# Kernel tuning notes

Hardware: AMD Instinct MI355X
Metric: run time of the kernel (lower is better)

The kernel has to match this reference:

```python
import jax, jax.numpy as jnp
import numpy as np

N, D, H = 4096, 1024, 16
DK = D // H

def setup_inputs() -> dict:
    key = jax.random.key(0)
    k1, k2 = jax.random.split(key)
    X = jax.random.normal(k1, (N, D), dtype=jnp.float32)
    # torch nn.Linear(D, 2D, bias=False): weight [2D, D]; y = x @ W.T. Store as [D, 2D].
    Wqkv = jax.random.normal(k2, (D, 2 * D), dtype=jnp.float32) * (1.0 / np.sqrt(D))
    return {"X": X, "Wqkv": Wqkv}

def reference(X, Wqkv):
    n = X.shape[0]
    proj = X @ Wqkv                      # [N, 2D]
    qk, v = jnp.split(proj, 2, axis=-1)  # each [N, D]
    qk = qk.reshape(n, H, DK)
    v = v.reshape(n, H, DK)
    scale = DK ** 0.5
    scores = jnp.einsum('nhd,mhd->hnm', qk, qk) / scale  # [H, N, N], Q == K
    att = jax.nn.softmax(scores, axis=-1)
    out = jnp.einsum('hnm,mhd->nhd', att, v)              # [N, H, DK]
    return out.reshape(n, D)
```

## Files before the change

kernel.cpp:

```cpp
#include <hip/hip_runtime.h>

typedef unsigned short u16;
typedef unsigned int u32;
typedef __bf16 bf16x8 __attribute__((ext_vector_type(8)));
typedef float f32x4 __attribute__((ext_vector_type(4)));
typedef float f32x16 __attribute__((ext_vector_type(16)));
typedef int i32x2 __attribute__((ext_vector_type(2)));
typedef unsigned int u32x4 __attribute__((ext_vector_type(4)));

#define N_TOK 4096
#define DMODEL 1024
#define NH 16
#define DKH 64

__device__ inline u16 f2bf(float f){
  unsigned u = __float_as_uint(f);
  u += 0x7fffu + ((u >> 16) & 1u);
  return (u16)(u >> 16);
}

__device__ inline float fexp2(float x){ return __builtin_amdgcn_exp2f(x); }

__global__ __launch_bounds__(256) void k_convX(const float* __restrict__ X, u16* __restrict__ Xb){
  int i = blockIdx.x*256 + threadIdx.x;
  const float4 v = reinterpret_cast<const float4*>(X)[i];
  ushort4 o; o.x=f2bf(v.x); o.y=f2bf(v.y); o.z=f2bf(v.z); o.w=f2bf(v.w);
  reinterpret_cast<ushort4*>(Xb)[i] = o;
}

__global__ __launch_bounds__(256) void k_convW(const float* __restrict__ W, u16* __restrict__ Wt){
  __shared__ float tile[64][65];
  const int bn = blockIdx.x*64;
  const int bk = blockIdx.y*64;
  const int t = threadIdx.x;
  const int c4 = (t & 15)*4;
  const int r  = t >> 4;
  #pragma unroll
  for (int i=0;i<4;i++){
    int k = r + i*16;
    const float4 v = *reinterpret_cast<const float4*>(&W[(size_t)(bk+k)*2048 + bn + c4]);
    tile[k][c4+0]=v.x; tile[k][c4+1]=v.y; tile[k][c4+2]=v.z; tile[k][c4+3]=v.w;
  }
  __syncthreads();
  #pragma unroll
  for (int i=0;i<4;i++){
    int n = r + i*16;
    ushort4 o;
    o.x = f2bf(tile[c4+0][n]);
    o.y = f2bf(tile[c4+1][n]);
    o.z = f2bf(tile[c4+2][n]);
    o.w = f2bf(tile[c4+3][n]);
    *reinterpret_cast<ushort4*>(&Wt[(size_t)(bn+n)*1024 + bk + c4]) = o;
  }
}

__global__ __launch_bounds__(256) void k_gemm(const u16* __restrict__ A, const u16* __restrict__ B,
                                              u16* __restrict__ kf_g, u16* __restrict__ vf_g){
  __shared__ alignas(16) u16 As[128*64];
  __shared__ alignas(16) u16 Bs[128*64];
  const int bm = blockIdx.y*128, bn = blockIdx.x*128;
  const int tid = threadIdx.x, wid = tid>>6, lane = tid&63;
  const int wr = wid>>1, wc = wid&1;
  const int lr = lane&15, lg = lane>>4;
  f32x4 acc[4][4] = {};

  for (int kk=0; kk<DMODEL; kk+=64){
    __syncthreads();
    #pragma unroll
    for (int i=0;i<4;i++){
      const int chunk = (wid*4+i)*64 + lane;
      const int row = chunk>>3, koc = chunk&7;
      const int swz = koc ^ (row&7);
      const u16* ga = A + (size_t)(bm+row)*DMODEL + kk + swz*8;
      const u16* gb = B + (size_t)(bn+row)*DMODEL + kk + swz*8;
      __builtin_amdgcn_global_load_lds((const __attribute__((address_space(1))) void*)ga,
          (__attribute__((address_space(3))) void*)(&As[(size_t)chunk*8]), 16, 0, 0);
      __builtin_amdgcn_global_load_lds((const __attribute__((address_space(1))) void*)gb,
          (__attribute__((address_space(3))) void*)(&Bs[(size_t)chunk*8]), 16, 0, 0);
    }
    asm volatile("s_waitcnt vmcnt(0)" ::: "memory");
    __syncthreads();
    #pragma unroll
    for (int ks=0; ks<2; ks++){
      bf16x8 af[4], bfr[4];
      #pragma unroll
      for (int m=0;m<4;m++){
        const int row = wr*64+m*16+lr, cr = ks*4+lg;
        af[m] = *reinterpret_cast<const bf16x8*>(&As[(size_t)(row*8 + (cr ^ (row&7)))*8]);
      }
      #pragma unroll
      for (int n=0;n<4;n++){
        const int row = wc*64+n*16+lr, cr = ks*4+lg;
        bfr[n] = *reinterpret_cast<const bf16x8*>(&Bs[(size_t)(row*8 + (cr ^ (row&7)))*8]);
      }
      #pragma unroll
      for (int m=0;m<4;m++)
        #pragma unroll
        for (int n=0;n<4;n++)
          acc[m][n] = __builtin_amdgcn_mfma_f32_16x16x32_bf16(af[m], bfr[n], acc[m][n], 0,0,0);
    }
  }

  #pragma unroll
  for (int m=0;m<4;m++){
    const int row0 = bm + wr*64 + m*16 + lg*4;
    #pragma unroll
    for (int n=0;n<4;n++){
      const int c = bn + wc*64 + n*16 + lr;
      if (c < DMODEL){
        const int hh = c>>6, d = c&63;
        const size_t base = ((size_t)hh*512 + (size_t)(row0>>5)*4 + (d>>4))*512;
        #pragma unroll
        for (int r=0;r<4;r++){
          const int row = row0 + r;
          kf_g[base + (size_t)(((row&31) | (((d>>3)&1)<<5)))*8 + (d&7)] = f2bf(acc[m][n][r]);
        }
      } else {
        const int cc = c - DMODEL; const int hh = cc>>6, d = cc&63;
        const size_t base = (((size_t)hh*64 + (row0>>6))*8 + (d>>5)*4 + ((row0>>4)&3))*512
                          + (size_t)(((d&31) | (((row0>>3)&1)<<5)))*8 + (row0&7);
        ushort4 o;
        o.x = f2bf(acc[m][n][0]); o.y = f2bf(acc[m][n][1]);
        o.z = f2bf(acc[m][n][2]); o.w = f2bf(acc[m][n][3]);
        *reinterpret_cast<ushort4*>(&vf_g[base]) = o;
      }
    }
  }
}

__device__ inline bf16x8 scale_bf8(bf16x8 v, float s){
  u32x4 w = __builtin_bit_cast(u32x4, v);
  u32x4 r;
  #pragma unroll
  for (int i=0;i<4;i++){
    float lo = __uint_as_float(w[i] << 16) * s;
    float hi = __uint_as_float(w[i] & 0xffff0000u) * s;
    u32 p;
    asm("v_cvt_pk_bf16_f32 %0, %1, %2" : "=v"(p) : "v"(lo), "v"(hi));
    r[i] = p;
  }
  return __builtin_bit_cast(bf16x8, r);
}

__global__ __launch_bounds__(256,3) void k_attn(const u16* __restrict__ kf_g, const u16* __restrict__ vf_g,
                                                float* __restrict__ out){
  __shared__ float comb[3][64][17];
  const int bid  = blockIdx.x;
  const int xcd  = bid & 7;
  const int slot = bid >> 3;
  const int h    = (xcd<<1) | (slot>>7);
  const int qt   = slot & 127;
  const int wid  = threadIdx.x >> 6;
  const int lane = threadIdx.x & 63;
  const int ql   = lane & 31;
  const int q0   = qt*32;
  const u16* __restrict__ Kfh = kf_g + (size_t)h*262144;
  const u16* __restrict__ Vfh = vf_g + (size_t)h*262144;
  const float SC = 0.18033688011112042f;

  bf16x8 qb[4];
  #pragma unroll
  for (int ds=0; ds<4; ds++){
    bf16x8 raw = *reinterpret_cast<const bf16x8*>(&Kfh[(size_t)((q0>>5)*4 + ds)*512 + lane*8]);
    qb[ds] = scale_bf8(raw, SC);
  }

  f32x16 o0 = {}, o1 = {};
  float lp = 0.f;
  const int kb = wid*1024;

  bf16x8 kf[8];
  auto loadKhalf = [&](int kt, int half){
    const u16* kp = Kfh + ((size_t)(kt>>5)*4)*512 + lane*8;
    #pragma unroll
    for (int fi=0; fi<4; fi++)
      kf[half*4+fi] = *reinterpret_cast<const bf16x8*>(kp + (size_t)(half*4+fi)*512);
  };

  auto body = [&](int kt, int ktn){
    const u16* vb = Vfh + ((size_t)(kt>>6)*8)*512 + lane*8;
    bf16x8 vf0[4], vf1[4];
    #pragma unroll
    for (int t=0; t<4; t++){
      vf0[t] = *reinterpret_cast<const bf16x8*>(vb + (size_t)t*512);
      vf1[t] = *reinterpret_cast<const bf16x8*>(vb + (size_t)(4+t)*512);
    }
    f32x16 p0 = {}, p1 = {};
    #pragma unroll
    for (int ds=0; ds<4; ds++) p0 = __builtin_amdgcn_mfma_f32_32x32x16_bf16(kf[ds],   qb[ds], p0, 0,0,0);
    loadKhalf(ktn, 0);
    #pragma unroll
    for (int ds=0; ds<4; ds++) p1 = __builtin_amdgcn_mfma_f32_32x32x16_bf16(kf[4+ds], qb[ds], p1, 0,0,0);
    loadKhalf(ktn, 1);

    #pragma unroll
    for (int c=0; c<16; c++){
      p0[c] = fexp2(p0[c]);
      p1[c] = fexp2(p1[c]);
    }
    {
      float r0 = ((p0[0]+p0[1])+(p0[2]+p0[3])) + ((p0[4]+p0[5])+(p0[6]+p0[7]));
      float r1 = ((p0[8]+p0[9])+(p0[10]+p0[11])) + ((p0[12]+p0[13])+(p0[14]+p0[15]));
      float r2 = ((p1[0]+p1[1])+(p1[2]+p1[3])) + ((p1[4]+p1[5])+(p1[6]+p1[7]));
      float r3 = ((p1[8]+p1[9])+(p1[10]+p1[11])) + ((p1[12]+p1[13])+(p1[14]+p1[15]));
      lp += (r0+r1)+(r2+r3);
    }

    u32 pk0[8], pk1[8];
    #pragma unroll
    for (int c2=0; c2<8; c2++){
      u32 a, b;
      asm("v_cvt_pk_bf16_f32 %0, %1, %2" : "=v"(a) : "v"(p0[2*c2]), "v"(p0[2*c2+1]));
      asm("v_cvt_pk_bf16_f32 %0, %1, %2" : "=v"(b) : "v"(p1[2*c2]), "v"(p1[2*c2+1]));
      pk0[c2] = a; pk1[c2] = b;
    }
    #pragma unroll
    for (int t=0; t<4; t++){
      const u32* pks = (t>>1) ? pk1 : pk0;
      const int base = 4*(t&1);
      i32x2 r0s = __builtin_amdgcn_permlane32_swap((int)pks[base+0], (int)pks[base+2], false, false);
      i32x2 r1s = __builtin_amdgcn_permlane32_swap((int)pks[base+1], (int)pks[base+3], false, false);
      u32x4 w; w[0] = (u32)r0s[0]; w[1] = (u32)r1s[0]; w[2] = (u32)r0s[1]; w[3] = (u32)r1s[1];
      bf16x8 bt = __builtin_bit_cast(bf16x8, w);
      o0 = __builtin_amdgcn_mfma_f32_32x32x16_bf16(vf0[t], bt, o0, 0,0,0);
      o1 = __builtin_amdgcn_mfma_f32_32x32x16_bf16(vf1[t], bt, o1, 0,0,0);
    }
  };

  loadKhalf(kb, 0); loadKhalf(kb, 1);
  for (int it=0; it<16; ++it){
    const int kt  = kb + (it<<6);
    const int ktn = kb + (((it+1)&15)<<6);
    body(kt, ktn);
  }

  lp += __shfl_xor(lp, 32, 64);

  if (wid){
    float* c = &comb[wid-1][lane][0];
    #pragma unroll
    for (int g=0; g<16; g++) c[g] = o0[g];
    c[16] = lp;
  }
  __syncthreads();
  if (!wid){
    #pragma unroll
    for (int w=0; w<3; w++){
      const float* c = &comb[w][lane][0];
      #pragma unroll
      for (int g=0; g<16; g++) o0[g] += c[g];
      lp += c[16];
    }
  }
  __syncthreads();
  if (wid){
    float* c = &comb[wid-1][lane][0];
    #pragma unroll
    for (int g=0; g<16; g++) c[g] = o1[g];
  }
  __syncthreads();
  if (!wid){
    #pragma unroll
    for (int w=0; w<3; w++){
      const float* c = &comb[w][lane][0];
      #pragma unroll
      for (int g=0; g<16; g++) o1[g] += c[g];
    }
    const int hi = lane >> 5;
    const float inv = 1.f / lp;
    float* orow = out + (size_t)(q0 + ql)*DMODEL + h*DKH;
    #pragma unroll
    for (int g=0; g<4; g++){
      float4 s0, s1;
      s0.x = o0[4*g+0]*inv; s0.y = o0[4*g+1]*inv; s0.z = o0[4*g+2]*inv; s0.w = o0[4*g+3]*inv;
      s1.x = o1[4*g+0]*inv; s1.y = o1[4*g+1]*inv; s1.z = o1[4*g+2]*inv; s1.w = o1[4*g+3]*inv;
      *reinterpret_cast<float4*>(&orow[      8*g + 4*hi]) = s0;
      *reinterpret_cast<float4*>(&orow[32 +  8*g + 4*hi]) = s1;
    }
  }
}

extern "C" void kernel_launch(void* const* d_in, const int* in_sizes, int n_in,
                              void* d_out, int out_size, void* d_ws, size_t ws_size,
                              hipStream_t stream) {
  const float* X = (const float*)d_in[0];
  const float* W = (const float*)d_in[1];
  float* out = (float*)d_out;
  u16* Xb = (u16*)d_ws;
  u16* Wt = Xb + (size_t)N_TOK*DMODEL;
  u16* Kf = Wt + (size_t)2*DMODEL*DMODEL;
  u16* Vf = Kf + (size_t)N_TOK*DMODEL;

  k_convX<<<dim3(4096), dim3(256), 0, stream>>>(X, Xb);
  k_convW<<<dim3(32,16), dim3(256), 0, stream>>>(W, Wt);
  k_gemm <<<dim3(16,32), dim3(256), 0, stream>>>(Xb, Wt, Kf, Vf);
  k_attn <<<dim3(2048), dim3(256), 0, stream>>>(Kf, Vf, out);
}
```

Measured before the change: 132.4 us.

## Replace software-pipelined 64-key loop with simple 32-key tile loop

The attention inner loop used to prefetch the next 64-key K tile into registers while computing the current one. It now walks 32-key tiles with loads issued at the top of each iteration and no explicit prefetch. This lowers register pressure and may raise occupancy or give the compiler more freedom in scheduling. The cost is that K/V load latency is no longer hidden explicitly and there are twice as many loop iterations.

```diff
diff --git a/kernel.cpp b/kernel.cpp
--- a/kernel.cpp
+++ b/kernel.cpp
@@ -169,69 +169,50 @@
   float lp = 0.f;
   const int kb = wid*1024;
 
-  bf16x8 kf[8];
-  auto loadKhalf = [&](int kt, int half){
+  for (int s=0; s<32; ++s){
+    const int kt = kb + s*32;
     const u16* kp = Kfh + ((size_t)(kt>>5)*4)*512 + lane*8;
-    #pragma unroll
-    for (int fi=0; fi<4; fi++)
-      kf[half*4+fi] = *reinterpret_cast<const bf16x8*>(kp + (size_t)(half*4+fi)*512);
-  };
-
-  auto body = [&](int kt, int ktn){
-    const u16* vb = Vfh + ((size_t)(kt>>6)*8)*512 + lane*8;
-    bf16x8 vf0[4], vf1[4];
-    #pragma unroll
-    for (int t=0; t<4; t++){
-      vf0[t] = *reinterpret_cast<const bf16x8*>(vb + (size_t)t*512);
-      vf1[t] = *reinterpret_cast<const bf16x8*>(vb + (size_t)(4+t)*512);
-    }
-    f32x16 p0 = {}, p1 = {};
-    #pragma unroll
-    for (int ds=0; ds<4; ds++) p0 = __builtin_amdgcn_mfma_f32_32x32x16_bf16(kf[ds],   qb[ds], p0, 0,0,0);
-    loadKhalf(ktn, 0);
-    #pragma unroll
-    for (int ds=0; ds<4; ds++) p1 = __builtin_amdgcn_mfma_f32_32x32x16_bf16(kf[4+ds], qb[ds], p1, 0,0,0);
-    loadKhalf(ktn, 1);
-
-    #pragma unroll
-    for (int c=0; c<16; c++){
-      p0[c] = fexp2(p0[c]);
-      p1[c] = fexp2(p1[c]);
-    }
+    bf16x8 kf0 = *reinterpret_cast<const bf16x8*>(kp);
+    bf16x8 kf1 = *reinterpret_cast<const bf16x8*>(kp + 512);
+    bf16x8 kf2 = *reinterpret_cast<const bf16x8*>(kp + 1024);
+    bf16x8 kf3 = *reinterpret_cast<const bf16x8*>(kp + 1536);
+    const u16* vb = Vfh + ((size_t)((kt>>6)*8 + (s&1)*2))*512 + lane*8;
+    bf16x8 va0 = *reinterpret_cast<const bf16x8*>(vb);
+    bf16x8 va1 = *reinterpret_cast<const bf16x8*>(vb + 512);
+    bf16x8 vb0 = *reinterpret_cast<const bf16x8*>(vb + 4*512);
+    bf16x8 vb1 = *reinterpret_cast<const bf16x8*>(vb + 5*512);
+
+    f32x16 p = {};
+    p = __builtin_amdgcn_mfma_f32_32x32x16_bf16(kf0, qb[0], p, 0,0,0);
+    p = __builtin_amdgcn_mfma_f32_32x32x16_bf16(kf1, qb[1], p, 0,0,0);
+    p = __builtin_amdgcn_mfma_f32_32x32x16_bf16(kf2, qb[2], p, 0,0,0);
+    p = __builtin_amdgcn_mfma_f32_32x32x16_bf16(kf3, qb[3], p, 0,0,0);
+
+    #pragma unroll
+    for (int c=0; c<16; c++) p[c] = fexp2(p[c]);
     {
-      float r0 = ((p0[0]+p0[1])+(p0[2]+p0[3])) + ((p0[4]+p0[5])+(p0[6]+p0[7]));
-      float r1 = ((p0[8]+p0[9])+(p0[10]+p0[11])) + ((p0[12]+p0[13])+(p0[14]+p0[15]));
-      float r2 = ((p1[0]+p1[1])+(p1[2]+p1[3])) + ((p1[4]+p1[5])+(p1[6]+p1[7]));
-      float r3 = ((p1[8]+p1[9])+(p1[10]+p1[11])) + ((p1[12]+p1[13])+(p1[14]+p1[15]));
-      lp += (r0+r1)+(r2+r3);
-    }
-
-    u32 pk0[8], pk1[8];
+      float r0 = ((p[0]+p[1])+(p[2]+p[3])) + ((p[4]+p[5])+(p[6]+p[7]));
+      float r1 = ((p[8]+p[9])+(p[10]+p[11])) + ((p[12]+p[13])+(p[14]+p[15]));
+      lp += r0+r1;
+    }
+
+    u32 pk[8];
     #pragma unroll
     for (int c2=0; c2<8; c2++){
-      u32 a, b;
-      asm("v_cvt_pk_bf16_f32 %0, %1, %2" : "=v"(a) : "v"(p0[2*c2]), "v"(p0[2*c2+1]));
-      asm("v_cvt_pk_bf16_f32 %0, %1, %2" : "=v"(b) : "v"(p1[2*c2]), "v"(p1[2*c2+1]));
-      pk0[c2] = a; pk1[c2] = b;
-    }
-    #pragma unroll
-    for (int t=0; t<4; t++){
-      const u32* pks = (t>>1) ? pk1 : pk0;
-      const int base = 4*(t&1);
-      i32x2 r0s = __builtin_amdgcn_permlane32_swap((int)pks[base+0], (int)pks[base+2], false, false);
-      i32x2 r1s = __builtin_amdgcn_permlane32_swap((int)pks[base+1], (int)pks[base+3], false, false);
+      u32 a;
+      asm("v_cvt_pk_bf16_f32 %0, %1, %2" : "=v"(a) : "v"(p[2*c2]), "v"(p[2*c2+1]));
+      pk[c2] = a;
+    }
+    #pragma unroll
+    for (int t2=0; t2<2; t2++){
+      const int base = 4*t2;
+      i32x2 r0s = __builtin_amdgcn_permlane32_swap((int)pk[base+0], (int)pk[base+2], false, false);
+      i32x2 r1s = __builtin_amdgcn_permlane32_swap((int)pk[base+1], (int)pk[base+3], false, false);
       u32x4 w; w[0] = (u32)r0s[0]; w[1] = (u32)r1s[0]; w[2] = (u32)r0s[1]; w[3] = (u32)r1s[1];
       bf16x8 bt = __builtin_bit_cast(bf16x8, w);
-      o0 = __builtin_amdgcn_mfma_f32_32x32x16_bf16(vf0[t], bt, o0, 0,0,0);
-      o1 = __builtin_amdgcn_mfma_f32_32x32x16_bf16(vf1[t], bt, o1, 0,0,0);
-    }
-  };
-
-  loadKhalf(kb, 0); loadKhalf(kb, 1);
-  for (int it=0; it<16; ++it){
-    const int kt  = kb + (it<<6);
-    const int ktn = kb + (((it+1)&15)<<6);
-    body(kt, ktn);
+      o0 = __builtin_amdgcn_mfma_f32_32x32x16_bf16(t2 ? va1 : va0, bt, o0, 0,0,0);
+      o1 = __builtin_amdgcn_mfma_f32_32x32x16_bf16(t2 ? vb1 : vb0, bt, o1, 0,0,0);
+    }
   }
 
   lp += __shfl_xor(lp, 32, 64);
```

New measurement: 133.4 us. About the same (+0.7%).
